# Performance work log

Hardware: AMD Instinct MI355X
Metric: run time of the kernel (lower is better)

## Reference

```python
import jax, jax.numpy as jnp
import numpy as np

N_NODES = 50000
N_EDGES = 1600000
D_IN = 512
D_OUT = 512


def setup_inputs() -> dict:
    key = jax.random.key(0)
    k1, k2, k3, k4, k5, k6 = jax.random.split(key, 6)
    stdv = 1.0 / np.sqrt(D_OUT)
    x = jax.random.normal(k1, (N_NODES, D_IN), dtype=jnp.float32)
    weight = jax.random.uniform(k2, (D_IN, D_OUT), dtype=jnp.float32, minval=-stdv, maxval=stdv)
    bias = jax.random.uniform(k3, (1, D_OUT), dtype=jnp.float32, minval=-stdv, maxval=stdv)
    edge_val = jax.random.uniform(k4, (N_EDGES,), dtype=jnp.float32)
    edge_row = jax.random.randint(k5, (N_EDGES,), 0, N_NODES, dtype=jnp.int64)
    edge_col = jax.random.randint(k6, (N_EDGES,), 0, N_NODES, dtype=jnp.int64)
    return {"x": x, "weight": weight, "bias": bias,
            "edge_val": edge_val, "edge_row": edge_row, "edge_col": edge_col}


def reference(x, weight, bias, edge_val, edge_row, edge_col):
    # hidden = X @ W  : [N, D_OUT] dense GEMM
    hidden = jnp.matmul(x, weight)
    # spmm: out[i] = sum over edges (i <- j) of adj_val * hidden[j]
    msgs = edge_val[:, None] * hidden[edge_col]            # [E, D_OUT]
    out = jax.ops.segment_sum(msgs, edge_row, num_segments=N_NODES)
    return out + bias
```

## Files before the change

kernel.cpp:

```cpp
#include <hip/hip_runtime.h>

typedef short short8 __attribute__((ext_vector_type(8)));
typedef float v4f   __attribute__((ext_vector_type(4)));

#define N_NODES 50000
#define N_EDGES 1600000
#define DIM     512
#define SCAN_NB 49

__device__ __forceinline__ float bf2f(unsigned short u) {
    unsigned int x = ((unsigned int)u) << 16;
    return __uint_as_float(x);
}
__device__ __forceinline__ unsigned int f2bfu(float f) {
    unsigned int x = __float_as_uint(f);
    unsigned int r = x + 0x7fffu + ((x >> 16) & 1u);
    return r >> 16;
}
__device__ __forceinline__ float lo16(unsigned int u) { return __uint_as_float(u << 16); }
__device__ __forceinline__ float hi16(unsigned int u) { return __uint_as_float(u & 0xffff0000u); }

__global__ void detect_kernel(const unsigned int* __restrict__ xw,
                              const int* __restrict__ erow,
                              int* __restrict__ flags) {
    __shared__ int cbf, cz;
    if (threadIdx.x == 0) { cbf = 0; cz = 0; }
    __syncthreads();
    int lb = 0, lz = 0;
    for (int i = threadIdx.x; i < 1024; i += 256) {
        unsigned int w = xw[i];
        unsigned int e0 = (w >> 7) & 0xFFu;
        unsigned int e1 = (w >> 23) & 0xFFu;
        if (e0 >= 0x70u && e0 <= 0x8Fu && e1 >= 0x70u && e1 <= 0x8Fu) lb++;
        if (erow[2 * i + 1] == 0) lz++;
    }
    atomicAdd(&cbf, lb);
    atomicAdd(&cz, lz);
    __syncthreads();
    if (threadIdx.x == 0) {
        flags[0] = (cbf > 512) ? 1 : 0;
        flags[1] = (cz > 512) ? 1 : 0;
    }
}

__global__ __launch_bounds__(256) void convert_x(const void* __restrict__ Xv,
                                                 unsigned short* __restrict__ Xc,
                                                 const int* __restrict__ flags) {
    if (flags[0] != 0) return;
    const float* Xf = (const float*)Xv;
    size_t i = ((size_t)blockIdx.x * 256 + threadIdx.x) * 8;
    float4 f0 = *(const float4*)(Xf + i);
    float4 f1 = *(const float4*)(Xf + i + 4);
    uint4 o;
    o.x = f2bfu(f0.x) | (f2bfu(f0.y) << 16);
    o.y = f2bfu(f0.z) | (f2bfu(f0.w) << 16);
    o.z = f2bfu(f1.x) | (f2bfu(f1.y) << 16);
    o.w = f2bfu(f1.z) | (f2bfu(f1.w) << 16);
    *(uint4*)(Xc + i) = o;
}

__global__ void transpose_w(const void* __restrict__ Wv,
                            unsigned short* __restrict__ Wt,
                            const int* __restrict__ flags) {
    __shared__ unsigned short tile[32][33];
    const bool fb = flags[0] != 0;
    int bx = blockIdx.x * 32, by = blockIdx.y * 32;
    int tx = threadIdx.x, ty = threadIdx.y;
    if (fb) {
        const unsigned short* W = (const unsigned short*)Wv;
        for (int r = ty; r < 32; r += 8)
            tile[r][tx] = W[(by + r) * DIM + bx + tx];
    } else {
        const float* W = (const float*)Wv;
        for (int r = ty; r < 32; r += 8)
            tile[r][tx] = (unsigned short)f2bfu(W[(by + r) * DIM + bx + tx]);
    }
    __syncthreads();
    for (int r = ty; r < 32; r += 8)
        Wt[(bx + r) * DIM + by + tx] = tile[tx][r];
}

#define TM 128
#define TN 128
#define BK 32
#define LP 40

__global__ __launch_bounds__(256) void gemm_kernel(
        const void* __restrict__ Xv,
        const unsigned short* __restrict__ Xc,
        const int have_xc,
        const unsigned short* __restrict__ Wt,
        unsigned short* __restrict__ H,
        const int* __restrict__ flags) {
    __shared__ unsigned short lA[TM * LP];
    __shared__ unsigned short lB[TN * LP];

    const bool fb = flags[0] != 0;
    const bool bfp = fb || (have_xc != 0);
    const unsigned short* Xb = fb ? (const unsigned short*)Xv : Xc;
    const float*          Xf = (const float*)Xv;

    const int t = threadIdx.x;
    const int mBase = blockIdx.y * TM;
    const int nBase = blockIdx.x * TN;
    const int w = t >> 6, lane = t & 63;
    const int lr = lane & 15, quad = lane >> 4;
    const int wr = w >> 1, wc = w & 1;

    v4f acc[4][4];
    #pragma unroll
    for (int i = 0; i < 4; ++i)
        #pragma unroll
        for (int j = 0; j < 4; ++j) acc[i][j] = (v4f)0.0f;

    for (int k0 = 0; k0 < DIM; k0 += BK) {
        #pragma unroll
        for (int rep = 0; rep < 2; ++rep) {
            int idx = rep * 256 + t;
            int r = idx >> 2;
            int cc = (idx & 3) * 8;
            int grow = mBase + r; if (grow >= N_NODES) grow = N_NODES - 1;
            size_t goff = (size_t)grow * DIM + k0 + cc;
            if (bfp) {
                uint4 av = *(const uint4*)(Xb + goff);
                *(uint4*)(&lA[r * LP + cc]) = av;
            } else {
                float4 a0 = *(const float4*)(Xf + goff);
                float4 a1 = *(const float4*)(Xf + goff + 4);
                uint4 av;
                av.x = f2bfu(a0.x) | (f2bfu(a0.y) << 16);
                av.y = f2bfu(a0.z) | (f2bfu(a0.w) << 16);
                av.z = f2bfu(a1.x) | (f2bfu(a1.y) << 16);
                av.w = f2bfu(a1.z) | (f2bfu(a1.w) << 16);
                *(uint4*)(&lA[r * LP + cc]) = av;
            }
            uint4 bv = *(const uint4*)(Wt + (size_t)(nBase + r) * DIM + k0 + cc);
            *(uint4*)(&lB[r * LP + cc]) = bv;
        }
        __syncthreads();

        short8 bfr[4];
        #pragma unroll
        for (int j = 0; j < 4; ++j)
            bfr[j] = *(const short8*)(&lB[(wc * 64 + j * 16 + lr) * LP + quad * 8]);
        #pragma unroll
        for (int i = 0; i < 4; ++i) {
            short8 a = *(const short8*)(&lA[(wr * 64 + i * 16 + lr) * LP + quad * 8]);
            #pragma unroll
            for (int j = 0; j < 4; ++j)
                acc[i][j] = __builtin_amdgcn_mfma_f32_16x16x32_bf16(a, bfr[j], acc[i][j], 0, 0, 0);
        }
        __syncthreads();
    }

    #pragma unroll
    for (int i = 0; i < 4; ++i) {
        #pragma unroll
        for (int j = 0; j < 4; ++j) {
            #pragma unroll
            for (int r = 0; r < 4; ++r) {
                int gm = mBase + wr * 64 + i * 16 + quad * 4 + r;
                int gn = nBase + wc * 64 + j * 16 + lr;
                if (gm < N_NODES)
                    H[(size_t)gm * DIM + gn] = (unsigned short)f2bfu(acc[i][j][r]);
            }
        }
    }
}

__global__ void hist_kernel(const int* __restrict__ row, int* __restrict__ cnt,
                            const int* __restrict__ flags) {
    const bool f64 = flags[1] != 0;
    int i = blockIdx.x * 256 + threadIdx.x;
    if (i < N_EDGES) {
        int r = f64 ? row[2 * (size_t)i] : row[i];
        atomicAdd(&cnt[r], 1);
    }
}

__global__ __launch_bounds__(256) void scan1_kernel(const int* __restrict__ cnt,
                                                    int* __restrict__ bsum) {
    __shared__ int sh[256];
    const int b = blockIdx.x, t = threadIdx.x;
    int base = b * 1024 + t * 4;
    int s = 0;
    #pragma unroll
    for (int k = 0; k < 4; ++k) {
        int i = base + k;
        if (i < N_NODES) s += cnt[i];
    }
    sh[t] = s;
    __syncthreads();
    for (int off = 128; off > 0; off >>= 1) {
        if (t < off) sh[t] += sh[t + off];
        __syncthreads();
    }
    if (t == 0) bsum[b] = sh[0];
}

__global__ __launch_bounds__(256) void scan3_kernel(const int* __restrict__ cnt,
                                                    const int* __restrict__ bsum,
                                                    int* __restrict__ start,
                                                    int* __restrict__ cursor) {
    __shared__ int sh[256];
    __shared__ int boffs;
    const int b = blockIdx.x, t = threadIdx.x;
    if (t == 0) {
        int r = 0;
        #pragma unroll 8
        for (int i = 0; i < b; ++i) r += bsum[i];
        boffs = r;
        if (b == 0) start[N_NODES] = N_EDGES;
    }
    int base = b * 1024 + t * 4;
    int v[4];
    #pragma unroll
    for (int k = 0; k < 4; ++k) {
        int i = base + k;
        v[k] = (i < N_NODES) ? cnt[i] : 0;
    }
    int tsum = v[0] + v[1] + v[2] + v[3];
    sh[t] = tsum;
    __syncthreads();
    for (int off = 1; off < 256; off <<= 1) {
        int x = (t >= off) ? sh[t - off] : 0;
        __syncthreads();
        sh[t] += x;
        __syncthreads();
    }
    int excl = sh[t] - tsum + boffs;
    #pragma unroll
    for (int k = 0; k < 4; ++k) {
        int i = base + k;
        if (i < N_NODES) { start[i] = excl; cursor[i] = excl; }
        excl += v[k];
    }
}

__global__ void scatter_kernel(const int* __restrict__ row, const int* __restrict__ col,
                               const void* __restrict__ valv,
                               int* __restrict__ cursor,
                               int2* __restrict__ sCV,
                               const int* __restrict__ flags) {
    const bool fb  = flags[0] != 0;
    const bool f64 = flags[1] != 0;
    int i = blockIdx.x * 256 + threadIdx.x;
    if (i < N_EDGES) {
        int r = f64 ? row[2 * (size_t)i] : row[i];
        int c = f64 ? col[2 * (size_t)i] : col[i];
        float v = fb ? bf2f(((const unsigned short*)valv)[i])
                     : ((const float*)valv)[i];
        int p = atomicAdd(&cursor[r], 1);
        int2 cv; cv.x = c; cv.y = __float_as_int(v);
        sCV[p] = cv;
    }
}

__global__ __launch_bounds__(256) void gather_kernel(
        const int* __restrict__ start, const int2* __restrict__ sCV,
        const unsigned short* __restrict__ H,
        const void* __restrict__ biasv, void* __restrict__ outv,
        const int* __restrict__ flags) {
    const bool fb = flags[0] != 0;
    const int lane = threadIdx.x & 63;
    const int node = blockIdx.x * 4 + (threadIdx.x >> 6);
    if (node >= N_NODES) return;
    const int s = start[node], e = start[node + 1];

    float a0 = 0.f, a1 = 0.f, a2 = 0.f, a3 = 0.f;
    float a4 = 0.f, a5 = 0.f, a6 = 0.f, a7 = 0.f;

    for (int p0 = s; p0 < e; p0 += 64) {
        int idx = p0 + lane;
        int clamped = (idx < e) ? idx : (e - 1);
        int2 cv = sCV[clamped];
        int cnt = e - p0; if (cnt > 64) cnt = 64;
        #pragma unroll 4
        for (int q = 0; q < cnt; ++q) {
            int col  = __builtin_amdgcn_readlane(cv.x, q);
            float v  = __int_as_float(__builtin_amdgcn_readlane(cv.y, q));
            uint4 h = *((const uint4*)(H + ((size_t)col << 9)) + lane);
            a0 = fmaf(v, lo16(h.x), a0);
            a1 = fmaf(v, hi16(h.x), a1);
            a2 = fmaf(v, lo16(h.y), a2);
            a3 = fmaf(v, hi16(h.y), a3);
            a4 = fmaf(v, lo16(h.z), a4);
            a5 = fmaf(v, hi16(h.z), a5);
            a6 = fmaf(v, lo16(h.w), a6);
            a7 = fmaf(v, hi16(h.w), a7);
        }
    }

    if (fb) {
        uint4 bb = *((const uint4*)biasv + lane);
        a0 += lo16(bb.x); a1 += hi16(bb.x);
        a2 += lo16(bb.y); a3 += hi16(bb.y);
        a4 += lo16(bb.z); a5 += hi16(bb.z);
        a6 += lo16(bb.w); a7 += hi16(bb.w);
        uint4 o;
        o.x = f2bfu(a0) | (f2bfu(a1) << 16);
        o.y = f2bfu(a2) | (f2bfu(a3) << 16);
        o.z = f2bfu(a4) | (f2bfu(a5) << 16);
        o.w = f2bfu(a6) | (f2bfu(a7) << 16);
        *((uint4*)((unsigned short*)outv + (size_t)node * DIM) + lane) = o;
    } else {
        const float4* bp = (const float4*)biasv + lane * 2;
        float4 b0 = bp[0], b1 = bp[1];
        float4 o0, o1;
        o0.x = a0 + b0.x; o0.y = a1 + b0.y; o0.z = a2 + b0.z; o0.w = a3 + b0.w;
        o1.x = a4 + b1.x; o1.y = a5 + b1.y; o1.z = a6 + b1.z; o1.w = a7 + b1.w;
        float4* op = (float4*)((float*)outv + (size_t)node * DIM) + lane * 2;
        op[0] = o0; op[1] = o1;
    }
}

extern "C" void kernel_launch(void* const* d_in, const int* in_sizes, int n_in,
                              void* d_out, int out_size, void* d_ws, size_t ws_size,
                              hipStream_t stream) {
    const void* X    = d_in[0];
    const void* W    = d_in[1];
    const void* bias = d_in[2];
    const void* eval = d_in[3];
    const int*  erow = (const int*)d_in[4];
    const int*  ecol = (const int*)d_in[5];

    char* w = (char*)d_ws;
    size_t o = 0;
    int* flags = (int*)(w + o); o += 256;
    unsigned short* hidden = (unsigned short*)(w + o); o += (size_t)N_NODES * DIM * 2;
    int2*  sCV    = (int2*)(w + o);  o += (size_t)N_EDGES * 8;
    int*   cnt    = (int*)(w + o);   o += 200704;
    int*   start  = (int*)(w + o);   o += 200704;
    int*   cursor = (int*)(w + o);   o += 200704;
    unsigned short* Wt = (unsigned short*)(w + o); o += (size_t)DIM * DIM * 2;
    int*   bsum   = (int*)(w + o);   o += 256;
    size_t base_end = o;
    unsigned short* Xc = (unsigned short*)(w + o);
    size_t need_xc = base_end + (size_t)N_NODES * DIM * 2;
    const int have_xc = (ws_size >= need_xc) ? 1 : 0;

    hipMemsetAsync(cnt, 0, N_NODES * sizeof(int), stream);

    detect_kernel<<<1, 256, 0, stream>>>((const unsigned int*)X, erow, flags);
    if (have_xc)
        convert_x<<<(N_NODES * DIM) / (256 * 8), 256, 0, stream>>>(X, Xc, flags);
    transpose_w<<<dim3(16, 16), dim3(32, 8), 0, stream>>>(W, Wt, flags);
    gemm_kernel<<<dim3(DIM / TN, (N_NODES + TM - 1) / TM), 256, 0, stream>>>(
        X, Xc, have_xc, Wt, hidden, flags);
    hist_kernel<<<(N_EDGES + 255) / 256, 256, 0, stream>>>(erow, cnt, flags);
    scan1_kernel<<<SCAN_NB, 256, 0, stream>>>(cnt, bsum);
    scan3_kernel<<<SCAN_NB, 256, 0, stream>>>(cnt, bsum, start, cursor);
    scatter_kernel<<<(N_EDGES + 255) / 256, 256, 0, stream>>>(erow, ecol, eval, cursor, sCV, flags);
    gather_kernel<<<(N_NODES + 3) / 4, 256, 0, stream>>>(start, sCV, hidden, bias, d_out, flags);
}
```

Measured before the change: 691.9 us.

## Use direct global-to-LDS loads in GEMM, sort edges per row, persistent gather

```diff
diff --git a/kernel.cpp b/kernel.cpp
--- a/kernel.cpp
+++ b/kernel.cpp
@@ -7,6 +7,7 @@
 #define N_EDGES 1600000
 #define DIM     512
 #define SCAN_NB 49
+#define GNB     2048
 
 __device__ __forceinline__ float bf2f(unsigned short u) {
     unsigned int x = ((unsigned int)u) << 16;
@@ -19,6 +20,20 @@
 }
 __device__ __forceinline__ float lo16(unsigned int u) { return __uint_as_float(u << 16); }
 __device__ __forceinline__ float hi16(unsigned int u) { return __uint_as_float(u & 0xffff0000u); }
+
+__device__ __forceinline__ unsigned long long shfl64_xor(unsigned long long v, int m) {
+    int lo = (int)(v & 0xffffffffull);
+    int hi = (int)(v >> 32);
+    lo = __shfl_xor(lo, m);
+    hi = __shfl_xor(hi, m);
+    return ((unsigned long long)(unsigned int)hi << 32) | (unsigned int)lo;
+}
+
+__device__ __forceinline__ void gload_lds16(const void* g, void* l) {
+    __builtin_amdgcn_global_load_lds(
+        (const __attribute__((address_space(1))) unsigned int*)g,
+        (__attribute__((address_space(3))) unsigned int*)l, 16, 0, 0);
+}
 
 __global__ void detect_kernel(const unsigned int* __restrict__ xw,
                               const int* __restrict__ erow,
@@ -83,7 +98,6 @@
 #define TM 128
 #define TN 128
 #define BK 32
-#define LP 40
 
 __global__ __launch_bounds__(256) void gemm_kernel(
         const void* __restrict__ Xv,
@@ -92,8 +106,8 @@
         const unsigned short* __restrict__ Wt,
         unsigned short* __restrict__ H,
         const int* __restrict__ flags) {
-    __shared__ unsigned short lA[TM * LP];
-    __shared__ unsigned short lB[TN * LP];
+    __shared__ unsigned short lA[TM * BK];
+    __shared__ unsigned short lB[TN * BK];
 
     const bool fb = flags[0] != 0;
     const bool bfp = fb || (have_xc != 0);
@@ -115,16 +129,29 @@
 
     for (int k0 = 0; k0 < DIM; k0 += BK) {
         #pragma unroll
-        for (int rep = 0; rep < 2; ++rep) {
-            int idx = rep * 256 + t;
-            int r = idx >> 2;
-            int cc = (idx & 3) * 8;
-            int grow = mBase + r; if (grow >= N_NODES) grow = N_NODES - 1;
-            size_t goff = (size_t)grow * DIM + k0 + cc;
-            if (bfp) {
-                uint4 av = *(const uint4*)(Xb + goff);
-                *(uint4*)(&lA[r * LP + cc]) = av;
-            } else {
+        for (int r = 0; r < 2; ++r) {
+            int chunk = w * 2 + r;
+            int row = chunk * 16 + (lane >> 2);
+            const unsigned short* gB = Wt + (size_t)(nBase + row) * DIM + k0 + (lane & 3) * 8;
+            gload_lds16(gB, lB + chunk * 512);
+        }
+        if (bfp) {
+            #pragma unroll
+            for (int r = 0; r < 2; ++r) {
+                int chunk = w * 2 + r;
+                int row = chunk * 16 + (lane >> 2);
+                int grow = mBase + row; if (grow >= N_NODES) grow = N_NODES - 1;
+                const unsigned short* gA = Xb + (size_t)grow * DIM + k0 + (lane & 3) * 8;
+                gload_lds16(gA, lA + chunk * 512);
+            }
+        } else {
+            #pragma unroll
+            for (int rep = 0; rep < 2; ++rep) {
+                int idx = rep * 256 + t;
+                int r = idx >> 2;
+                int cc = (idx & 3) * 8;
+                int grow = mBase + r; if (grow >= N_NODES) grow = N_NODES - 1;
+                size_t goff = (size_t)grow * DIM + k0 + cc;
                 float4 a0 = *(const float4*)(Xf + goff);
                 float4 a1 = *(const float4*)(Xf + goff + 4);
                 uint4 av;
@@ -132,20 +159,18 @@
                 av.y = f2bfu(a0.z) | (f2bfu(a0.w) << 16);
                 av.z = f2bfu(a1.x) | (f2bfu(a1.y) << 16);
                 av.w = f2bfu(a1.z) | (f2bfu(a1.w) << 16);
-                *(uint4*)(&lA[r * LP + cc]) = av;
-            }
-            uint4 bv = *(const uint4*)(Wt + (size_t)(nBase + r) * DIM + k0 + cc);
-            *(uint4*)(&lB[r * LP + cc]) = bv;
+                *(uint4*)(&lA[r * BK + cc]) = av;
+            }
         }
         __syncthreads();
 
         short8 bfr[4];
         #pragma unroll
         for (int j = 0; j < 4; ++j)
-            bfr[j] = *(const short8*)(&lB[(wc * 64 + j * 16 + lr) * LP + quad * 8]);
+            bfr[j] = *(const short8*)(&lB[(wc * 64 + j * 16 + lr) * BK + quad * 8]);
         #pragma unroll
         for (int i = 0; i < 4; ++i) {
-            short8 a = *(const short8*)(&lA[(wr * 64 + i * 16 + lr) * LP + quad * 8]);
+            short8 a = *(const short8*)(&lA[(wr * 64 + i * 16 + lr) * BK + quad * 8]);
             #pragma unroll
             for (int j = 0; j < 4; ++j)
                 acc[i][j] = __builtin_amdgcn_mfma_f32_16x16x32_bf16(a, bfr[j], acc[i][j], 0, 0, 0);
@@ -173,7 +198,7 @@
     const bool f64 = flags[1] != 0;
     int i = blockIdx.x * 256 + threadIdx.x;
     if (i < N_EDGES) {
-        int r = f64 ? row[2 * (size_t)i] : row[i];
+        int r = f64 ? ((const int2*)row)[i].x : row[i];
         atomicAdd(&cnt[r], 1);
     }
 }
@@ -246,8 +271,8 @@
     const bool f64 = flags[1] != 0;
     int i = blockIdx.x * 256 + threadIdx.x;
     if (i < N_EDGES) {
-        int r = f64 ? row[2 * (size_t)i] : row[i];
-        int c = f64 ? col[2 * (size_t)i] : col[i];
+        int r = f64 ? ((const int2*)row)[i].x : row[i];
+        int c = f64 ? ((const int2*)col)[i].x : col[i];
         float v = fb ? bf2f(((const unsigned short*)valv)[i])
                      : ((const float*)valv)[i];
         int p = atomicAdd(&cursor[r], 1);
@@ -256,61 +281,88 @@
     }
 }
 
-__global__ __launch_bounds__(256) void gather_kernel(
+__global__ __launch_bounds__(256, 8) void gather_kernel(
         const int* __restrict__ start, const int2* __restrict__ sCV,
         const unsigned short* __restrict__ H,
         const void* __restrict__ biasv, void* __restrict__ outv,
         const int* __restrict__ flags) {
     const bool fb = flags[0] != 0;
     const int lane = threadIdx.x & 63;
-    const int node = blockIdx.x * 4 + (threadIdx.x >> 6);
-    if (node >= N_NODES) return;
-    const int s = start[node], e = start[node + 1];
-
-    float a0 = 0.f, a1 = 0.f, a2 = 0.f, a3 = 0.f;
-    float a4 = 0.f, a5 = 0.f, a6 = 0.f, a7 = 0.f;
-
-    for (int p0 = s; p0 < e; p0 += 64) {
-        int idx = p0 + lane;
-        int clamped = (idx < e) ? idx : (e - 1);
-        int2 cv = sCV[clamped];
-        int cnt = e - p0; if (cnt > 64) cnt = 64;
-        #pragma unroll 4
-        for (int q = 0; q < cnt; ++q) {
-            int col  = __builtin_amdgcn_readlane(cv.x, q);
-            float v  = __int_as_float(__builtin_amdgcn_readlane(cv.y, q));
-            uint4 h = *((const uint4*)(H + ((size_t)col << 9)) + lane);
-            a0 = fmaf(v, lo16(h.x), a0);
-            a1 = fmaf(v, hi16(h.x), a1);
-            a2 = fmaf(v, lo16(h.y), a2);
-            a3 = fmaf(v, hi16(h.y), a3);
-            a4 = fmaf(v, lo16(h.z), a4);
-            a5 = fmaf(v, hi16(h.z), a5);
-            a6 = fmaf(v, lo16(h.w), a6);
-            a7 = fmaf(v, hi16(h.w), a7);
-        }
-    }
-
+    const int wv = threadIdx.x >> 6;
+
+    float b0v = 0, b1v = 0, b2v = 0, b3v = 0, b4v = 0, b5v = 0, b6v = 0, b7v = 0;
     if (fb) {
         uint4 bb = *((const uint4*)biasv + lane);
-        a0 += lo16(bb.x); a1 += hi16(bb.x);
-        a2 += lo16(bb.y); a3 += hi16(bb.y);
-        a4 += lo16(bb.z); a5 += hi16(bb.z);
-        a6 += lo16(bb.w); a7 += hi16(bb.w);
-        uint4 o;
-        o.x = f2bfu(a0) | (f2bfu(a1) << 16);
-        o.y = f2bfu(a2) | (f2bfu(a3) << 16);
-        o.z = f2bfu(a4) | (f2bfu(a5) << 16);
-        o.w = f2bfu(a6) | (f2bfu(a7) << 16);
-        *((uint4*)((unsigned short*)outv + (size_t)node * DIM) + lane) = o;
+        b0v = lo16(bb.x); b1v = hi16(bb.x);
+        b2v = lo16(bb.y); b3v = hi16(bb.y);
+        b4v = lo16(bb.z); b5v = hi16(bb.z);
+        b6v = lo16(bb.w); b7v = hi16(bb.w);
     } else {
         const float4* bp = (const float4*)biasv + lane * 2;
-        float4 b0 = bp[0], b1 = bp[1];
-        float4 o0, o1;
-        o0.x = a0 + b0.x; o0.y = a1 + b0.y; o0.z = a2 + b0.z; o0.w = a3 + b0.w;
-        o1.x = a4 + b1.x; o1.y = a5 + b1.y; o1.z = a6 + b1.z; o1.w = a7 + b1.w;
-        float4* op = (float4*)((float*)outv + (size_t)node * DIM) + lane * 2;
-        op[0] = o0; op[1] = o1;
+        float4 f0 = bp[0], f1 = bp[1];
+        b0v = f0.x; b1v = f0.y; b2v = f0.z; b3v = f0.w;
+        b4v = f1.x; b5v = f1.y; b6v = f1.z; b7v = f1.w;
+    }
+
+    for (int node = blockIdx.x * 4 + wv; node < N_NODES; node += GNB * 4) {
+        const int s = start[node], e = start[node + 1];
+
+        float a0 = 0.f, a1 = 0.f, a2 = 0.f, a3 = 0.f;
+        float a4 = 0.f, a5 = 0.f, a6 = 0.f, a7 = 0.f;
+
+        for (int p0 = s; p0 < e; p0 += 64) {
+            int idx = p0 + lane;
+            unsigned long long key;
+            if (idx < e) {
+                int2 cv = sCV[idx];
+                key = ((unsigned long long)(unsigned int)cv.x << 32) | (unsigned int)cv.y;
+            } else {
+                key = ~0ull;
+            }
+            #pragma unroll
+            for (int k = 2; k <= 64; k <<= 1) {
+                #pragma unroll
+                for (int j = k >> 1; j > 0; j >>= 1) {
+                    unsigned long long other = shfl64_xor(key, j);
+                    bool keep_min = (((lane & j) == 0) == ((lane & k) == 0));
+                    unsigned long long mn = (key < other) ? key : other;
+                    unsigned long long mx = (key < other) ? other : key;
+                    key = keep_min ? mn : mx;
+                }
+            }
+            int cnt = e - p0; if (cnt > 64) cnt = 64;
+            int klo = (int)(key & 0xffffffffull);
+            int khi = (int)(key >> 32);
+            #pragma unroll 4
+            for (int q = 0; q < cnt; ++q) {
+                int col  = __builtin_amdgcn_readlane(khi, q);
+                float v  = __int_as_float(__builtin_amdgcn_readlane(klo, q));
+                uint4 h = *((const uint4*)(H + ((size_t)(unsigned int)col << 9)) + lane);
+                a0 = fmaf(v, lo16(h.x), a0);
+                a1 = fmaf(v, hi16(h.x), a1);
+                a2 = fmaf(v, lo16(h.y), a2);
+                a3 = fmaf(v, hi16(h.y), a3);
+                a4 = fmaf(v, lo16(h.z), a4);
+                a5 = fmaf(v, hi16(h.z), a5);
+                a6 = fmaf(v, lo16(h.w), a6);
+                a7 = fmaf(v, hi16(h.w), a7);
+            }
+        }
+
+        if (fb) {
+            uint4 o;
+            o.x = f2bfu(a0 + b0v) | (f2bfu(a1 + b1v) << 16);
+            o.y = f2bfu(a2 + b2v) | (f2bfu(a3 + b3v) << 16);
+            o.z = f2bfu(a4 + b4v) | (f2bfu(a5 + b5v) << 16);
+            o.w = f2bfu(a6 + b6v) | (f2bfu(a7 + b7v) << 16);
+            *((uint4*)((unsigned short*)outv + (size_t)node * DIM) + lane) = o;
+        } else {
+            float4 o0, o1;
+            o0.x = a0 + b0v; o0.y = a1 + b1v; o0.z = a2 + b2v; o0.w = a3 + b3v;
+            o1.x = a4 + b4v; o1.y = a5 + b5v; o1.z = a6 + b6v; o1.w = a7 + b7v;
+            float4* op = (float4*)((float*)outv + (size_t)node * DIM) + lane * 2;
+            op[0] = o0; op[1] = o1;
+        }
     }
 }
 
@@ -351,5 +403,5 @@
     scan1_kernel<<<SCAN_NB, 256, 0, stream>>>(cnt, bsum);
     scan3_kernel<<<SCAN_NB, 256, 0, stream>>>(cnt, bsum, start, cursor);
     scatter_kernel<<<(N_EDGES + 255) / 256, 256, 0, stream>>>(erow, ecol, eval, cursor, sCV, flags);
-    gather_kernel<<<(N_NODES + 3) / 4, 256, 0, stream>>>(start, sCV, hidden, bias, d_out, flags);
-}
+    gather_kernel<<<GNB, 256, 0, stream>>>(start, sCV, hidden, bias, d_out, flags);
+}
```

After: 672.5 us. 2.8% less time.
